# Optimization experiments

Measured on AMD Instinct MI355X. Metric: run time of the kernel, lower is better.

## Reference

```python
import jax, jax.numpy as jnp
from jax import lax
import numpy as np

B = 128          # batch size
S = 207          # input spatial size implied by outputSpatialSize=[8,8]
N_PTS = 256000
NEG = -1e30      # -inf stand-in for masked max-pooling
# BNReLU channel counts in execution order: 8 resnet blocks x (bn1, bn2), final resnet BN(32), last BN(64)
SIZES = [8,8,8,8,8,16,16,16,16,24,24,24,24,32,32,32,32,64]
OFF = np.cumsum([0] + SIZES)

WSHAPES = dict(conv0=(3,3,1,8),
               c1a=(3,3,8,8), c1b=(3,3,8,8), c2a=(3,3,8,8), c2b=(3,3,8,8),
               c3a=(3,3,8,16), c3b=(3,3,16,16), c3r=(3,3,8,16),
               c4a=(3,3,16,16), c4b=(3,3,16,16),
               c5a=(3,3,16,24), c5b=(3,3,24,24), c5r=(3,3,16,24),
               c6a=(3,3,24,24), c6b=(3,3,24,24),
               c7a=(3,3,24,32), c7b=(3,3,32,32), c7r=(3,3,24,32),
               c8a=(3,3,32,32), c8b=(3,3,32,32),
               conv_last=(5,5,32,64))

def _conv(x, w, stride, padding):
    return lax.conv_general_dilated(x, w, (stride, stride), padding,
                                    dimension_numbers=('NHWC', 'HWIO', 'NHWC'))

def _pool_max(x, win, stride, init):
    return lax.reduce_window(x, init, lax.max, (1, win, win, 1), (1, stride, stride, 1), 'VALID')

def _bnrelu(x, m, g, b):
    # eval-mode BN folded to affine, applied on active sites only (inactive stay exactly 0)
    return m * jax.nn.relu(x * g + b)

def _subconv(x, w, m):
    # submanifold conv == dense conv on zero-filled grid, output restricted to active sites
    return _conv(x, w, 1, 'SAME') * m

def _strided(x, w, m, win, stride):
    # scn.Convolution: output site active iff any active input in its receptive field
    m2 = _pool_max(m, win, stride, 0.0)
    return _conv(x, w, stride, 'VALID') * m2, m2

def _block(x, m, g1, b1, w1, g2, b2, w2, wres, stride):
    # pre-activation basic block from scn.SparseResNet
    h = _bnrelu(x, m, g1, b1)
    if stride == 1:
        h, m2 = _subconv(h, w1, m), m
    else:
        h, m2 = _strided(h, w1, m, 3, 2)
    h = _subconv(_bnrelu(h, m2, g2, b2), w2, m2)
    r = x if wres is None else _strided(x, wres, m, 3, 2)[0]
    return h + r, m2

def _forward(locations, batch_idx, features, bn_gamma, bn_beta, W):
    idx = (batch_idx, locations[:, 0], locations[:, 1], jnp.zeros_like(batch_idx))
    x = jnp.zeros((B, S, S, 1), jnp.float32).at[idx].add(features[:, 0])  # InputLayer (sum dups)
    m = jnp.zeros((B, S, S, 1), jnp.float32).at[idx].set(1.0)             # active-site mask
    g = [bn_gamma[OFF[i]:OFF[i+1]] for i in range(len(SIZES))]
    b = [bn_beta[OFF[i]:OFF[i+1]] for i in range(len(SIZES))]
    x = _subconv(x, W['conv0'], m)                              # 1->8 @ 207x207
    # MaxPooling(pool 3, stride 2) over active sites only
    m2 = _pool_max(m, 3, 2, 0.0)
    x = jnp.where(m2 > 0, _pool_max(jnp.where(m > 0, x, NEG), 3, 2, NEG), 0.0)
    m = m2                                                      # @ 103x103
    blocks = [('c1a', 'c1b', None, 1), ('c2a', 'c2b', None, 1),
              ('c3a', 'c3b', 'c3r', 2), ('c4a', 'c4b', None, 1),
              ('c5a', 'c5b', 'c5r', 2), ('c6a', 'c6b', None, 1),
              ('c7a', 'c7b', 'c7r', 2), ('c8a', 'c8b', None, 1)]
    for i, (k1, k2, kr, st) in enumerate(blocks):
        x, m = _block(x, m, g[2*i], b[2*i], W[k1], g[2*i+1], b[2*i+1], W[k2],
                      None if kr is None else W[kr], st)        # 103->51->25->12
    x = _bnrelu(x, m, g[16], b[16])                             # final resnet BNReLU(32)
    x, m = _strided(x, W['conv_last'], m, 5, 1)                 # 32->64, 12x12 -> 8x8
    x = _bnrelu(x, m, g[17], b[17])
    flat = x.transpose(0, 3, 1, 2).reshape(B, -1)               # SparseToDense + flatten (NCHW order)
    return (flat @ W['w_lin'].T).reshape(B, -1, 1)              # [B, 100, 1]

def setup_inputs():
    key = jax.random.key(0)
    ks = iter(jax.random.split(key, 64))
    inp = {
        'locations': jax.random.randint(next(ks), (N_PTS, 2), 0, S, dtype=jnp.int32),
        'batch_idx': jax.random.randint(next(ks), (N_PTS,), 0, B, dtype=jnp.int32),
        'features': jax.random.normal(next(ks), (N_PTS, 1), jnp.float32),
        'bn_gamma': 1.0 + 0.1 * jax.random.normal(next(ks), (int(OFF[-1]),), jnp.float32),
        'bn_beta': 0.1 * jax.random.normal(next(ks), (int(OFF[-1]),), jnp.float32),
    }
    for name, shp in WSHAPES.items():
        fan_in = int(np.prod(shp[:-1]))
        inp[name] = jax.random.normal(next(ks), shp, jnp.float32) * (2.0 / fan_in) ** 0.5
    inp['w_lin'] = jax.random.normal(next(ks), (100, 64 * 8 * 8), jnp.float32) * (1.0 / 4096.0) ** 0.5
    return inp

def reference(locations, batch_idx, features, bn_gamma, bn_beta, conv0,
              c1a, c1b, c2a, c2b, c3a, c3b, c3r, c4a, c4b, c5a, c5b, c5r,
              c6a, c6b, c7a, c7b, c7r, c8a, c8b, conv_last, w_lin):
    W = dict(conv0=conv0, c1a=c1a, c1b=c1b, c2a=c2a, c2b=c2b, c3a=c3a, c3b=c3b, c3r=c3r,
             c4a=c4a, c4b=c4b, c5a=c5a, c5b=c5b, c5r=c5r, c6a=c6a, c6b=c6b,
             c7a=c7a, c7b=c7b, c7r=c7r, c8a=c8a, c8b=c8b, conv_last=conv_last, w_lin=w_lin)
    return _forward(locations, batch_idx, features, bn_gamma, bn_beta, W)
```

## Files before the change

kernel.cpp:

```cpp
#include <hip/hip_runtime.h>

#define S 207
#define BATCH 128
#define NPTS 256000

static const int OFFS[19] = {0,8,16,24,32,40,56,72,88,104,128,152,176,200,232,264,296,328,392};

__global__ void zero2_kernel(float4* __restrict__ a, float4* __restrict__ b, int n4) {
    int i = blockIdx.x * blockDim.x + threadIdx.x;
    if (i < n4) { a[i] = make_float4(0,0,0,0); b[i] = make_float4(0,0,0,0); }
}

__global__ void zero_kernel(float* __restrict__ p, int n) {
    int i = blockIdx.x * blockDim.x + threadIdx.x;
    if (i < n) p[i] = 0.0f;
}

__global__ void scatter_kernel(const int* __restrict__ loc, const int* __restrict__ bidx,
                               const float* __restrict__ feat,
                               float* __restrict__ xs, float* __restrict__ ms) {
    int t = blockIdx.x * blockDim.x + threadIdx.x;
    if (t >= NPTS) return;
    int b = bidx[t];
    int r = loc[2 * t];
    int c = loc[2 * t + 1];
    int idx = (b * S + r) * S + c;
    atomicAdd(&xs[idx], feat[t]);
    ms[idx] = 1.0f;
}

__global__ __launch_bounds__(256) void conv0_pool_kernel(
    const float* __restrict__ xs, const float* __restrict__ ms,
    const float* __restrict__ w,
    float* __restrict__ x1, float* __restrict__ m1) {
    const int Hout = 103;
    int opix = blockIdx.x * 256 + threadIdx.x;
    int total = BATCH * Hout * Hout;
    if (opix >= total) return;
    int wo = opix % Hout;
    int t = opix / Hout;
    int ho = t % Hout;
    int b  = t / Hout;

    float mv[3][3];
    float mwin = 0.0f;
    #pragma unroll
    for (int pi = 0; pi < 3; ++pi)
        #pragma unroll
        for (int pj = 0; pj < 3; ++pj) {
            float m = ms[(b * S + 2 * ho + pi) * S + 2 * wo + pj];
            mv[pi][pj] = m;
            mwin = fmaxf(mwin, m);
        }
    float* xp = x1 + (size_t)opix * 8;
    if (mwin <= 0.0f) {
        *(float4*)xp = make_float4(0,0,0,0);
        *(float4*)(xp + 4) = make_float4(0,0,0,0);
        m1[opix] = 0.0f;
        return;
    }
    float p[5][5];
    #pragma unroll
    for (int r = 0; r < 5; ++r) {
        int ii = 2 * ho - 1 + r;
        #pragma unroll
        for (int c = 0; c < 5; ++c) {
            int jj = 2 * wo - 1 + c;
            bool ok = ((unsigned)ii < (unsigned)S) && ((unsigned)jj < (unsigned)S);
            p[r][c] = ok ? xs[(b * S + ii) * S + jj] : 0.0f;
        }
    }
    float best[8];
    #pragma unroll
    for (int co = 0; co < 8; ++co) best[co] = -1e30f;
    #pragma unroll
    for (int pi = 0; pi < 3; ++pi)
        #pragma unroll
        for (int pj = 0; pj < 3; ++pj) {
            if (mv[pi][pj] > 0.0f) {
                float acc[8];
                #pragma unroll
                for (int co = 0; co < 8; ++co) acc[co] = 0.0f;
                #pragma unroll
                for (int kh = 0; kh < 3; ++kh)
                    #pragma unroll
                    for (int kw = 0; kw < 3; ++kw) {
                        float x = p[pi + kh][pj + kw];
                        #pragma unroll
                        for (int co = 0; co < 8; ++co)
                            acc[co] = fmaf(x, w[(kh * 3 + kw) * 8 + co], acc[co]);
                    }
                #pragma unroll
                for (int co = 0; co < 8; ++co) best[co] = fmaxf(best[co], acc[co]);
            }
        }
    *(float4*)xp = make_float4(best[0], best[1], best[2], best[3]);
    *(float4*)(xp + 4) = make_float4(best[4], best[5], best[6], best[7]);
    m1[opix] = 1.0f;
}

template <int C, int TILE, int NTX>
__global__ __launch_bounds__(256) void resblock_kernel(
    const float* __restrict__ in, const float* __restrict__ mask,
    const float* __restrict__ w1, const float* __restrict__ w2,
    const float* __restrict__ g1, const float* __restrict__ bb1,
    const float* __restrict__ g2, const float* __restrict__ bb2,
    float* __restrict__ out, int H) {
    constexpr int XT = TILE + 4, HT = TILE + 2;
    constexpr int XA = XT * XT, HA = HT * HT;
    __shared__ float xs[C][XA];
    __shared__ float h1[C][HA];
    __shared__ float msh[XA];

    int tid = threadIdx.x;
    int bid = blockIdx.x;
    int b = bid / (NTX * NTX);
    int t = bid % (NTX * NTX);
    int r0 = (t / NTX) * TILE, c0 = (t % NTX) * TILE;

    float gr[C], br[C];
    #pragma unroll
    for (int c = 0; c < C; ++c) { gr[c] = g1[c]; br[c] = bb1[c]; }

    for (int i = tid; i < XA; i += 256) {
        int py = i / XT, px = i % XT;
        int gy = r0 - 2 + py, gx = c0 - 2 + px;
        bool ok = (unsigned)gy < (unsigned)H && (unsigned)gx < (unsigned)H;
        float m = 0.0f;
        if (ok) m = mask[(size_t)(b * H + gy) * H + gx];
        msh[i] = m;
        if (m > 0.0f) {
            const float* ip = in + ((size_t)(b * H + gy) * H + gx) * C;
            #pragma unroll
            for (int c = 0; c < C; ++c)
                xs[c][i] = m * fmaxf(fmaf(ip[c], gr[c], br[c]), 0.0f);
        } else {
            #pragma unroll
            for (int c = 0; c < C; ++c) xs[c][i] = 0.0f;
        }
    }
    #pragma unroll
    for (int c = 0; c < C; ++c) { gr[c] = g2[c]; br[c] = bb2[c]; }
    __syncthreads();

    for (int pos = tid; pos < HA; pos += 256) {
        int py = pos / HT, px = pos % HT;
        float mc = msh[(py + 1) * XT + px + 1];
        float acc[C];
        #pragma unroll
        for (int co = 0; co < C; ++co) acc[co] = 0.0f;
        if (mc > 0.0f) {
            #pragma unroll
            for (int kh = 0; kh < 3; ++kh)
                #pragma unroll
                for (int kw = 0; kw < 3; ++kw) {
                    int pix = (py + kh) * XT + px + kw;
                    const float* wp = w1 + (kh * 3 + kw) * C * C;
                    #pragma unroll
                    for (int ci = 0; ci < C; ++ci) {
                        float xv = xs[ci][pix];
                        #pragma unroll
                        for (int co = 0; co < C; ++co)
                            acc[co] = fmaf(xv, wp[ci * C + co], acc[co]);
                    }
                }
        }
        #pragma unroll
        for (int co = 0; co < C; ++co)
            h1[co][pos] = mc * fmaxf(fmaf(acc[co] * mc, gr[co], br[co]), 0.0f);
    }
    __syncthreads();

    {
        int ty = tid / TILE, tx = tid % TILE;
        int gy = r0 + ty, gx = c0 + tx;
        if (gy < H && gx < H) {
            float mo = msh[(ty + 2) * XT + tx + 2];
            float acc[C];
            #pragma unroll
            for (int co = 0; co < C; ++co) acc[co] = 0.0f;
            if (mo > 0.0f) {
                #pragma unroll
                for (int kh = 0; kh < 3; ++kh)
                    #pragma unroll
                    for (int kw = 0; kw < 3; ++kw) {
                        int pix = (ty + kh) * HT + tx + kw;
                        const float* wp = w2 + (kh * 3 + kw) * C * C;
                        #pragma unroll
                        for (int ci = 0; ci < C; ++ci) {
                            float xv = h1[ci][pix];
                            #pragma unroll
                            for (int co = 0; co < C; ++co)
                                acc[co] = fmaf(xv, wp[ci * C + co], acc[co]);
                        }
                    }
            }
            const float* rp = in + ((size_t)(b * H + gy) * H + gx) * C;
            float* op = out + ((size_t)(b * H + gy) * H + gx) * C;
            #pragma unroll
            for (int j = 0; j < C; j += 4) {
                float4 r4 = *(const float4*)(rp + j);
                float4 o4;
                o4.x = fmaf(acc[j],     mo, r4.x);
                o4.y = fmaf(acc[j + 1], mo, r4.y);
                o4.z = fmaf(acc[j + 2], mo, r4.z);
                o4.w = fmaf(acc[j + 3], mo, r4.w);
                *(float4*)(op + j) = o4;
            }
        }
    }
}

template <int K, int CIN, int COUT, int COT, bool BN, bool RES>
__global__ __launch_bounds__(256) void fconv_kernel(
    const float* __restrict__ in, const float* __restrict__ w,
    const float* __restrict__ g, const float* __restrict__ bbn,
    const float* __restrict__ mIn, const float* __restrict__ mOut,
    const float* __restrict__ res, float* __restrict__ out,
    int Hin, int Hout, int stride, int pad) {
    const int Win = Hin, Wout = Hout;
    int npix = BATCH * Hout * Wout;
    int opix = blockIdx.x * 256 + threadIdx.x;
    if (opix >= npix) return;
    int co0 = blockIdx.y * COT;
    int wo = opix % Wout;
    int t = opix / Wout;
    int ho = t % Hout;
    int b  = t / Hout;

    float mo = mOut[opix];
    float* op = out + (size_t)opix * COUT + co0;
    if (mo <= 0.0f) {
        #pragma unroll
        for (int j = 0; j < COT; j += 4) {
            float4 r4 = RES ? *(const float4*)(res + (size_t)opix * COUT + co0 + j)
                            : make_float4(0,0,0,0);
            *(float4*)(op + j) = r4;
        }
        return;
    }
    float acc[COT];
    #pragma unroll
    for (int j = 0; j < COT; ++j) acc[j] = 0.0f;

    #pragma unroll
    for (int kh = 0; kh < K; ++kh) {
        int ih = ho * stride + kh - pad;
        if ((unsigned)ih >= (unsigned)Hin) continue;
        #pragma unroll
        for (int kw = 0; kw < K; ++kw) {
            int iw = wo * stride + kw - pad;
            if ((unsigned)iw >= (unsigned)Win) continue;
            int ipix = (b * Hin + ih) * Win + iw;
            float mi = 1.0f;
            if (BN) { mi = mIn[ipix]; if (mi <= 0.0f) continue; }
            const float* ip = in + (size_t)ipix * CIN;
            const float* wp = w + (kh * K + kw) * CIN * COUT + co0;
            #pragma unroll
            for (int ci = 0; ci < CIN; ci += 4) {
                float4 xv = *(const float4*)(ip + ci);
                if (BN) {
                    xv.x = mi * fmaxf(fmaf(xv.x, g[ci],     bbn[ci]),     0.0f);
                    xv.y = mi * fmaxf(fmaf(xv.y, g[ci + 1], bbn[ci + 1]), 0.0f);
                    xv.z = mi * fmaxf(fmaf(xv.z, g[ci + 2], bbn[ci + 2]), 0.0f);
                    xv.w = mi * fmaxf(fmaf(xv.w, g[ci + 3], bbn[ci + 3]), 0.0f);
                }
                #pragma unroll
                for (int j = 0; j < COT; ++j) {
                    acc[j] = fmaf(xv.x, wp[(ci    ) * COUT + j], acc[j]);
                    acc[j] = fmaf(xv.y, wp[(ci + 1) * COUT + j], acc[j]);
                    acc[j] = fmaf(xv.z, wp[(ci + 2) * COUT + j], acc[j]);
                    acc[j] = fmaf(xv.w, wp[(ci + 3) * COUT + j], acc[j]);
                }
            }
        }
    }
    #pragma unroll
    for (int j = 0; j < COT; j += 4) {
        float4 o4;
        o4.x = acc[j] * mo; o4.y = acc[j+1] * mo; o4.z = acc[j+2] * mo; o4.w = acc[j+3] * mo;
        if (RES) {
            float4 r4 = *(const float4*)(res + (size_t)opix * COUT + co0 + j);
            o4.x += r4.x; o4.y += r4.y; o4.z += r4.z; o4.w += r4.w;
        }
        *(float4*)(op + j) = o4;
    }
}

template <int CIN, int COUT, int COT>
__global__ __launch_bounds__(256) void strided_ra_kernel(
    const float* __restrict__ in,
    const float* __restrict__ wR, const float* __restrict__ wA,
    const float* __restrict__ g, const float* __restrict__ bbn,
    const float* __restrict__ mIn, float* __restrict__ mOutBuf,
    float* __restrict__ outR, float* __restrict__ outA,
    int Hin, int Hout) {
    constexpr int NG = COUT / COT;
    int npix = BATCH * Hout * Hout;
    int opix = blockIdx.x * 256 + threadIdx.x;
    if (opix >= npix) return;
    int path = blockIdx.y / NG;
    int co0  = (blockIdx.y % NG) * COT;
    int wo = opix % Hout;
    int t = opix / Hout;
    int ho = t % Hout;
    int b  = t / Hout;

    const float* wsel = path ? wA : wR;
    float acc[COT];
    #pragma unroll
    for (int j = 0; j < COT; ++j) acc[j] = 0.0f;
    float m2 = 0.0f;

    #pragma unroll
    for (int kh = 0; kh < 3; ++kh) {
        int ih = 2 * ho + kh;
        #pragma unroll
        for (int kw = 0; kw < 3; ++kw) {
            int iw = 2 * wo + kw;
            int ipix = (b * Hin + ih) * Hin + iw;
            float mi = mIn[ipix];
            if (mi <= 0.0f) continue;
            m2 = fmaxf(m2, mi);
            const float* ip = in + (size_t)ipix * CIN;
            const float* wp = wsel + (kh * 3 + kw) * CIN * COUT + co0;
            #pragma unroll
            for (int ci = 0; ci < CIN; ci += 4) {
                float4 xv = *(const float4*)(ip + ci);
                if (path) {
                    xv.x = mi * fmaxf(fmaf(xv.x, g[ci],     bbn[ci]),     0.0f);
                    xv.y = mi * fmaxf(fmaf(xv.y, g[ci + 1], bbn[ci + 1]), 0.0f);
                    xv.z = mi * fmaxf(fmaf(xv.z, g[ci + 2], bbn[ci + 2]), 0.0f);
                    xv.w = mi * fmaxf(fmaf(xv.w, g[ci + 3], bbn[ci + 3]), 0.0f);
                }
                #pragma unroll
                for (int j = 0; j < COT; ++j) {
                    acc[j] = fmaf(xv.x, wp[(ci    ) * COUT + j], acc[j]);
                    acc[j] = fmaf(xv.y, wp[(ci + 1) * COUT + j], acc[j]);
                    acc[j] = fmaf(xv.z, wp[(ci + 2) * COUT + j], acc[j]);
                    acc[j] = fmaf(xv.w, wp[(ci + 3) * COUT + j], acc[j]);
                }
            }
        }
    }
    if (blockIdx.y == 0) mOutBuf[opix] = m2;
    float* op = (path ? outA : outR) + (size_t)opix * COUT + co0;
    #pragma unroll
    for (int j = 0; j < COT; j += 4) {
        float4 o4;
        o4.x = acc[j] * m2; o4.y = acc[j+1] * m2; o4.z = acc[j+2] * m2; o4.w = acc[j+3] * m2;
        *(float4*)(op + j) = o4;
    }
}

__global__ void pool_kernel(const float* __restrict__ in, float* __restrict__ out,
                            int Hin, int Win, int Hout, int Wout, int win, int stride) {
    int tid = blockIdx.x * blockDim.x + threadIdx.x;
    int total = BATCH * Hout * Wout;
    if (tid >= total) return;
    int wo = tid % Wout;
    int p = tid / Wout;
    int ho = p % Hout;
    int b  = p / Hout;
    float mx = 0.0f;
    for (int i = 0; i < win; ++i)
        for (int j = 0; j < win; ++j)
            mx = fmaxf(mx, in[(b * Hin + ho * stride + i) * Win + wo * stride + j]);
    out[tid] = mx;
}

__global__ __launch_bounds__(256) void bn_tr_kernel(
    const float* __restrict__ x, const float* __restrict__ m,
    const float* __restrict__ g, const float* __restrict__ bb,
    float* __restrict__ xt) {
    int tid = blockIdx.x * 256 + threadIdx.x;
    if (tid >= BATCH * 4096) return;
    int c = tid & 63, hw = (tid >> 6) & 63, b = tid >> 12;
    float v = m[b * 64 + hw] * fmaxf(fmaf(x[tid], g[c], bb[c]), 0.0f);
    xt[((size_t)b << 12) + c * 64 + hw] = v;
}

__global__ __launch_bounds__(256) void linear_gemm_kernel(
    const float* __restrict__ xt, const float* __restrict__ wl,
    float* __restrict__ out) {
    int o = blockIdx.x;
    int half = threadIdx.x >> 7;
    int b = threadIdx.x & 127;
    int k0 = blockIdx.y * 512 + half * 256;
    const float* xp = xt + ((size_t)b << 12) + k0;
    const float* wp = wl + o * 4096 + k0;
    float acc = 0.0f;
    #pragma unroll 16
    for (int k = 0; k < 256; k += 4) {
        float4 xv = *(const float4*)(xp + k);
        float4 wv = *(const float4*)(wp + k);
        acc = fmaf(xv.x, wv.x, acc); acc = fmaf(xv.y, wv.y, acc);
        acc = fmaf(xv.z, wv.z, acc); acc = fmaf(xv.w, wv.w, acc);
    }
    atomicAdd(&out[b * 100 + o], acc);
}

template <int K, int CIN, int COUT, int COT, bool BN, bool RES>
static inline void fconv(hipStream_t s, const float* in, const float* w,
                         const float* g, const float* bbn,
                         const float* mIn, const float* mOut, const float* res,
                         float* out, int Hin, int Hout, int stride, int pad) {
    int npix = BATCH * Hout * Hout;
    dim3 grid((npix + 255) / 256, COUT / COT);
    fconv_kernel<K, CIN, COUT, COT, BN, RES><<<grid, 256, 0, s>>>(
        in, w, g, bbn, mIn, mOut, res, out, Hin, Hout, stride, pad);
}

template <int CIN, int COUT, int COT>
static inline void strided_ra(hipStream_t s, const float* in, const float* wR, const float* wA,
                              const float* g, const float* bbn, const float* mIn,
                              float* mOutBuf, float* outR, float* outA, int Hin, int Hout) {
    int npix = BATCH * Hout * Hout;
    dim3 grid((npix + 255) / 256, 2 * (COUT / COT));
    strided_ra_kernel<CIN, COUT, COT><<<grid, 256, 0, s>>>(
        in, wR, wA, g, bbn, mIn, mOutBuf, outR, outA, Hin, Hout);
}

extern "C" void kernel_launch(void* const* d_in, const int* in_sizes, int n_in,
                              void* d_out, int out_size, void* d_ws, size_t ws_size,
                              hipStream_t stream) {
    const int*   loc   = (const int*)d_in[0];
    const int*   bidx  = (const int*)d_in[1];
    const float* feat  = (const float*)d_in[2];
    const float* gamma = (const float*)d_in[3];
    const float* beta  = (const float*)d_in[4];
    const float* Wconv0 = (const float*)d_in[5];
    const float* Wc1a = (const float*)d_in[6];
    const float* Wc1b = (const float*)d_in[7];
    const float* Wc2a = (const float*)d_in[8];
    const float* Wc2b = (const float*)d_in[9];
    const float* Wc3a = (const float*)d_in[10];
    const float* Wc3b = (const float*)d_in[11];
    const float* Wc3r = (const float*)d_in[12];
    const float* Wc4a = (const float*)d_in[13];
    const float* Wc4b = (const float*)d_in[14];
    const float* Wc5a = (const float*)d_in[15];
    const float* Wc5b = (const float*)d_in[16];
    const float* Wc5r = (const float*)d_in[17];
    const float* Wc6a = (const float*)d_in[18];
    const float* Wc6b = (const float*)d_in[19];
    const float* Wc7a = (const float*)d_in[20];
    const float* Wc7b = (const float*)d_in[21];
    const float* Wc7r = (const float*)d_in[22];
    const float* Wc8a = (const float*)d_in[23];
    const float* Wc8b = (const float*)d_in[24];
    const float* Wlast = (const float*)d_in[25];
    const float* wlin  = (const float*)d_in[26];

    const size_t SZB = (size_t)BATCH * 103 * 103 * 8;
    const size_t SZM = (size_t)BATCH * 103 * 103;
    float* b0 = (float*)d_ws;
    float* b1 = b0 + SZB;
    float* b2 = b1 + SZB;
    float* m0 = b2 + SZB;
    float* m1 = m0 + SZM;

    const float* G[18];
    const float* Bt[18];
    for (int i = 0; i < 18; ++i) { G[i] = gamma + OFFS[i]; Bt[i] = beta + OFFS[i]; }

    {
        int n = BATCH * S * S;
        zero2_kernel<<<(n / 4 + 255) / 256, 256, 0, stream>>>((float4*)b1, (float4*)b2, n / 4);
        scatter_kernel<<<(NPTS + 255) / 256, 256, 0, stream>>>(loc, bidx, feat, b1, b2);
        int total = BATCH * 103 * 103;
        conv0_pool_kernel<<<(total + 255) / 256, 256, 0, stream>>>(b1, b2, Wconv0, b0, m0);
    }

    resblock_kernel<8, 16, 7><<<dim3(7 * 7 * BATCH), 256, 0, stream>>>(
        b0, m0, Wc1a, Wc1b, G[0], Bt[0], G[1], Bt[1], b1, 103);
    resblock_kernel<8, 16, 7><<<dim3(7 * 7 * BATCH), 256, 0, stream>>>(
        b1, m0, Wc2a, Wc2b, G[2], Bt[2], G[3], Bt[3], b2, 103);
    strided_ra<8, 16, 16>(stream, b2, Wc3r, Wc3a, G[4], Bt[4], m0, m1, b0, b1, 103, 51);
    fconv<3, 16, 16, 8, true, true >(stream, b1, Wc3b, G[5], Bt[5], m1, m1, b0, b2, 51, 51, 1, 1);
    fconv<3, 16, 16, 8, true, false>(stream, b2, Wc4a, G[6], Bt[6], m1, m1, nullptr, b0, 51, 51, 1, 1);
    fconv<3, 16, 16, 8, true, true >(stream, b0, Wc4b, G[7], Bt[7], m1, m1, b2,      b1, 51, 51, 1, 1);
    strided_ra<16, 24, 24>(stream, b1, Wc5r, Wc5a, G[8], Bt[8], m1, m0, b0, b2, 51, 25);
    fconv<3, 24, 24, 8, true, true >(stream, b2, Wc5b, G[9], Bt[9], m0, m0, b0, b1, 25, 25, 1, 1);
    fconv<3, 24, 24, 8, true, false>(stream, b1, Wc6a, G[10], Bt[10], m0, m0, nullptr, b0, 25, 25, 1, 1);
    fconv<3, 24, 24, 8, true, true >(stream, b0, Wc6b, G[11], Bt[11], m0, m0, b1,      b2, 25, 25, 1, 1);
    strided_ra<24, 32, 8>(stream, b2, Wc7r, Wc7a, G[12], Bt[12], m0, m1, b0, b1, 25, 12);
    fconv<3, 32, 32, 4, true, true >(stream, b1, Wc7b, G[13], Bt[13], m1, m1, b0, b2, 12, 12, 1, 1);
    fconv<3, 32, 32, 4, true, false>(stream, b2, Wc8a, G[14], Bt[14], m1, m1, nullptr, b0, 12, 12, 1, 1);
    fconv<3, 32, 32, 4, true, true >(stream, b0, Wc8b, G[15], Bt[15], m1, m1, b2,      b1, 12, 12, 1, 1);
    pool_kernel<<<(BATCH * 64 + 255) / 256, 256, 0, stream>>>(m1, m0, 12, 12, 8, 8, 5, 1);
    fconv<5, 32, 64, 4, true, false>(stream, b1, Wlast, G[16], Bt[16], m1, m0, nullptr, b0, 12, 8, 1, 0);
    bn_tr_kernel<<<(BATCH * 4096 + 255) / 256, 256, 0, stream>>>(b0, m0, G[17], Bt[17], b2);
    zero_kernel<<<(BATCH * 100 + 255) / 256, 256, 0, stream>>>((float*)d_out, BATCH * 100);
    linear_gemm_kernel<<<dim3(100, 8), 256, 0, stream>>>(b2, wlin, (float*)d_out);
}
```

Before: 797.3 us.

## Batch conv input loads per row and add shared-memory tiled last conv

The generic and strided conv kernels now issue all input loads for a kernel row before computing, and use predicated zeroing instead of early continues, which gives more memory-level parallelism at the cost of more registers. The final 5x5 conv is replaced by a dedicated kernel that stages BN-ReLU'd input rows and weights in shared memory, split by kernel row across blocks. Its partial sums go to a buffer that the BN/transpose kernel reduces. The 51x51 layers also switch to a full 16-channel output tile, which removes redundant input reads. Trade-offs are the loads now issued for inactive neighbours, the larger partial buffer traffic, and some lost occupancy.

```diff
diff --git a/kernel.cpp b/kernel.cpp
--- a/kernel.cpp
+++ b/kernel.cpp
@@ -246,31 +246,52 @@
     #pragma unroll
     for (int kh = 0; kh < K; ++kh) {
         int ih = ho * stride + kh - pad;
-        if ((unsigned)ih >= (unsigned)Hin) continue;
+        bool rok = (unsigned)ih < (unsigned)Hin;
+        int ihc = rok ? ih : 0;
+        float mi[K];
+        float4 xv[K][CIN / 4];
         #pragma unroll
         for (int kw = 0; kw < K; ++kw) {
             int iw = wo * stride + kw - pad;
-            if ((unsigned)iw >= (unsigned)Win) continue;
-            int ipix = (b * Hin + ih) * Win + iw;
-            float mi = 1.0f;
-            if (BN) { mi = mIn[ipix]; if (mi <= 0.0f) continue; }
+            bool ok = rok && ((unsigned)iw < (unsigned)Win);
+            int ipix = (b * Hin + ihc) * Win + (ok ? iw : 0);
+            float m = mIn[ipix];
+            mi[kw] = ok ? m : 0.0f;
             const float* ip = in + (size_t)ipix * CIN;
+            #pragma unroll
+            for (int q = 0; q < CIN / 4; ++q) xv[kw][q] = *(const float4*)(ip + 4 * q);
+        }
+        #pragma unroll
+        for (int kw = 0; kw < K; ++kw) {
+            if (BN) {
+                bool on = mi[kw] > 0.0f;
+                #pragma unroll
+                for (int q = 0; q < CIN / 4; ++q) {
+                    int ci = 4 * q;
+                    float4& x4 = xv[kw][q];
+                    x4.x = on ? fmaxf(fmaf(x4.x, g[ci],     bbn[ci]),     0.0f) : 0.0f;
+                    x4.y = on ? fmaxf(fmaf(x4.y, g[ci + 1], bbn[ci + 1]), 0.0f) : 0.0f;
+                    x4.z = on ? fmaxf(fmaf(x4.z, g[ci + 2], bbn[ci + 2]), 0.0f) : 0.0f;
+                    x4.w = on ? fmaxf(fmaf(x4.w, g[ci + 3], bbn[ci + 3]), 0.0f) : 0.0f;
+                }
+            } else {
+                bool on = mi[kw] > 0.0f;
+                if (!on) {
+                    #pragma unroll
+                    for (int q = 0; q < CIN / 4; ++q) xv[kw][q] = make_float4(0,0,0,0);
+                }
+            }
             const float* wp = w + (kh * K + kw) * CIN * COUT + co0;
             #pragma unroll
-            for (int ci = 0; ci < CIN; ci += 4) {
-                float4 xv = *(const float4*)(ip + ci);
-                if (BN) {
-                    xv.x = mi * fmaxf(fmaf(xv.x, g[ci],     bbn[ci]),     0.0f);
-                    xv.y = mi * fmaxf(fmaf(xv.y, g[ci + 1], bbn[ci + 1]), 0.0f);
-                    xv.z = mi * fmaxf(fmaf(xv.z, g[ci + 2], bbn[ci + 2]), 0.0f);
-                    xv.w = mi * fmaxf(fmaf(xv.w, g[ci + 3], bbn[ci + 3]), 0.0f);
-                }
+            for (int q = 0; q < CIN / 4; ++q) {
+                float4 x4 = xv[kw][q];
+                int ci = 4 * q;
                 #pragma unroll
                 for (int j = 0; j < COT; ++j) {
-                    acc[j] = fmaf(xv.x, wp[(ci    ) * COUT + j], acc[j]);
-                    acc[j] = fmaf(xv.y, wp[(ci + 1) * COUT + j], acc[j]);
-                    acc[j] = fmaf(xv.z, wp[(ci + 2) * COUT + j], acc[j]);
-                    acc[j] = fmaf(xv.w, wp[(ci + 3) * COUT + j], acc[j]);
+                    acc[j] = fmaf(x4.x, wp[(ci    ) * COUT + j], acc[j]);
+                    acc[j] = fmaf(x4.y, wp[(ci + 1) * COUT + j], acc[j]);
+                    acc[j] = fmaf(x4.z, wp[(ci + 2) * COUT + j], acc[j]);
+                    acc[j] = fmaf(x4.w, wp[(ci + 3) * COUT + j], acc[j]);
                 }
             }
         }
@@ -315,30 +336,44 @@
     #pragma unroll
     for (int kh = 0; kh < 3; ++kh) {
         int ih = 2 * ho + kh;
+        float mi[3];
+        float4 xv[3][CIN / 4];
         #pragma unroll
         for (int kw = 0; kw < 3; ++kw) {
             int iw = 2 * wo + kw;
             int ipix = (b * Hin + ih) * Hin + iw;
-            float mi = mIn[ipix];
-            if (mi <= 0.0f) continue;
-            m2 = fmaxf(m2, mi);
+            mi[kw] = mIn[ipix];
             const float* ip = in + (size_t)ipix * CIN;
+            #pragma unroll
+            for (int q = 0; q < CIN / 4; ++q) xv[kw][q] = *(const float4*)(ip + 4 * q);
+        }
+        #pragma unroll
+        for (int kw = 0; kw < 3; ++kw) {
+            float m = mi[kw];
+            m2 = fmaxf(m2, m);
+            if (path) {
+                bool on = m > 0.0f;
+                #pragma unroll
+                for (int q = 0; q < CIN / 4; ++q) {
+                    int ci = 4 * q;
+                    float4& x4 = xv[kw][q];
+                    x4.x = on ? fmaxf(fmaf(x4.x, g[ci],     bbn[ci]),     0.0f) : 0.0f;
+                    x4.y = on ? fmaxf(fmaf(x4.y, g[ci + 1], bbn[ci + 1]), 0.0f) : 0.0f;
+                    x4.z = on ? fmaxf(fmaf(x4.z, g[ci + 2], bbn[ci + 2]), 0.0f) : 0.0f;
+                    x4.w = on ? fmaxf(fmaf(x4.w, g[ci + 3], bbn[ci + 3]), 0.0f) : 0.0f;
+                }
+            }
             const float* wp = wsel + (kh * 3 + kw) * CIN * COUT + co0;
             #pragma unroll
-            for (int ci = 0; ci < CIN; ci += 4) {
-                float4 xv = *(const float4*)(ip + ci);
-                if (path) {
-                    xv.x = mi * fmaxf(fmaf(xv.x, g[ci],     bbn[ci]),     0.0f);
-                    xv.y = mi * fmaxf(fmaf(xv.y, g[ci + 1], bbn[ci + 1]), 0.0f);
-                    xv.z = mi * fmaxf(fmaf(xv.z, g[ci + 2], bbn[ci + 2]), 0.0f);
-                    xv.w = mi * fmaxf(fmaf(xv.w, g[ci + 3], bbn[ci + 3]), 0.0f);
-                }
+            for (int q = 0; q < CIN / 4; ++q) {
+                float4 x4 = xv[kw][q];
+                int ci = 4 * q;
                 #pragma unroll
                 for (int j = 0; j < COT; ++j) {
-                    acc[j] = fmaf(xv.x, wp[(ci    ) * COUT + j], acc[j]);
-                    acc[j] = fmaf(xv.y, wp[(ci + 1) * COUT + j], acc[j]);
-                    acc[j] = fmaf(xv.z, wp[(ci + 2) * COUT + j], acc[j]);
-                    acc[j] = fmaf(xv.w, wp[(ci + 3) * COUT + j], acc[j]);
+                    acc[j] = fmaf(x4.x, wp[(ci    ) * COUT + j], acc[j]);
+                    acc[j] = fmaf(x4.y, wp[(ci + 1) * COUT + j], acc[j]);
+                    acc[j] = fmaf(x4.z, wp[(ci + 2) * COUT + j], acc[j]);
+                    acc[j] = fmaf(x4.w, wp[(ci + 3) * COUT + j], acc[j]);
                 }
             }
         }
@@ -351,6 +386,78 @@
         o4.x = acc[j] * m2; o4.y = acc[j+1] * m2; o4.z = acc[j+2] * m2; o4.w = acc[j+3] * m2;
         *(float4*)(op + j) = o4;
     }
+}
+
+__global__ __launch_bounds__(256) void convlast_kernel(
+    const float* __restrict__ in,
+    const float* __restrict__ w,
+    const float* __restrict__ g, const float* __restrict__ bb,
+    const float* __restrict__ mIn,
+    float* __restrict__ part) {
+    __shared__ float xs[32 * 97];
+    __shared__ float ws[5 * 32 * 64];
+    int b   = blockIdx.x;
+    int kh  = blockIdx.y;
+    int tid = threadIdx.x;
+    for (int i = tid; i < 8 * 12 * 32; i += 256) {
+        int ci = i & 31;
+        int p  = i >> 5;
+        int gpix = (b * 12 + kh + p / 12) * 12 + (p % 12);
+        float m = mIn[gpix];
+        float v = 0.0f;
+        if (m > 0.0f) v = fmaxf(fmaf(in[(size_t)gpix * 32 + ci], g[ci], bb[ci]), 0.0f);
+        xs[ci * 97 + p] = v;
+    }
+    {
+        const float4* src = (const float4*)(w + kh * (5 * 32 * 64));
+        float4* dst = (float4*)ws;
+        for (int i = tid; i < 5 * 32 * 64 / 4; i += 256) dst[i] = src[i];
+    }
+    __syncthreads();
+
+    int px = tid & 63;
+    int cg = tid >> 6;
+    int ho = px >> 3, wo = px & 7;
+    float acc[16];
+    #pragma unroll
+    for (int j = 0; j < 16; ++j) acc[j] = 0.0f;
+    #pragma unroll
+    for (int kw = 0; kw < 5; ++kw) {
+        const float* xp = xs + ho * 12 + wo + kw;
+        const float* wp = ws + kw * (32 * 64) + cg * 16;
+        #pragma unroll
+        for (int ci = 0; ci < 32; ++ci) {
+            float xv = xp[ci * 97];
+            const float* wr = wp + ci * 64;
+            #pragma unroll
+            for (int j = 0; j < 16; j += 4) {
+                float4 w4 = *(const float4*)(wr + j);
+                acc[j]     = fmaf(xv, w4.x, acc[j]);
+                acc[j + 1] = fmaf(xv, w4.y, acc[j + 1]);
+                acc[j + 2] = fmaf(xv, w4.z, acc[j + 2]);
+                acc[j + 3] = fmaf(xv, w4.w, acc[j + 3]);
+            }
+        }
+    }
+    float* op = part + ((((size_t)kh * BATCH + b) * 64 + px) * 64) + cg * 16;
+    #pragma unroll
+    for (int j = 0; j < 16; j += 4)
+        *(float4*)(op + j) = make_float4(acc[j], acc[j+1], acc[j+2], acc[j+3]);
+}
+
+__global__ __launch_bounds__(256) void bn_tr_kernel(
+    const float* __restrict__ part, const float* __restrict__ m,
+    const float* __restrict__ g, const float* __restrict__ bb,
+    float* __restrict__ xt) {
+    int tid = blockIdx.x * 256 + threadIdx.x;
+    if (tid >= BATCH * 4096) return;
+    int c = tid & 63, hw = (tid >> 6) & 63, b = tid >> 12;
+    float s = 0.0f;
+    #pragma unroll
+    for (int k = 0; k < 5; ++k)
+        s += part[(((size_t)k * BATCH + b) * 64 + hw) * 64 + c];
+    float v = m[b * 64 + hw] * fmaxf(fmaf(s, g[c], bb[c]), 0.0f);
+    xt[((size_t)b << 12) + c * 64 + hw] = v;
 }
 
 __global__ void pool_kernel(const float* __restrict__ in, float* __restrict__ out,
@@ -367,17 +474,6 @@
         for (int j = 0; j < win; ++j)
             mx = fmaxf(mx, in[(b * Hin + ho * stride + i) * Win + wo * stride + j]);
     out[tid] = mx;
-}
-
-__global__ __launch_bounds__(256) void bn_tr_kernel(
-    const float* __restrict__ x, const float* __restrict__ m,
-    const float* __restrict__ g, const float* __restrict__ bb,
-    float* __restrict__ xt) {
-    int tid = blockIdx.x * 256 + threadIdx.x;
-    if (tid >= BATCH * 4096) return;
-    int c = tid & 63, hw = (tid >> 6) & 63, b = tid >> 12;
-    float v = m[b * 64 + hw] * fmaxf(fmaf(x[tid], g[c], bb[c]), 0.0f);
-    xt[((size_t)b << 12) + c * 64 + hw] = v;
 }
 
 __global__ __launch_bounds__(256) void linear_gemm_kernel(
@@ -477,9 +573,9 @@
     resblock_kernel<8, 16, 7><<<dim3(7 * 7 * BATCH), 256, 0, stream>>>(
         b1, m0, Wc2a, Wc2b, G[2], Bt[2], G[3], Bt[3], b2, 103);
     strided_ra<8, 16, 16>(stream, b2, Wc3r, Wc3a, G[4], Bt[4], m0, m1, b0, b1, 103, 51);
-    fconv<3, 16, 16, 8, true, true >(stream, b1, Wc3b, G[5], Bt[5], m1, m1, b0, b2, 51, 51, 1, 1);
-    fconv<3, 16, 16, 8, true, false>(stream, b2, Wc4a, G[6], Bt[6], m1, m1, nullptr, b0, 51, 51, 1, 1);
-    fconv<3, 16, 16, 8, true, true >(stream, b0, Wc4b, G[7], Bt[7], m1, m1, b2,      b1, 51, 51, 1, 1);
+    fconv<3, 16, 16, 16, true, true >(stream, b1, Wc3b, G[5], Bt[5], m1, m1, b0, b2, 51, 51, 1, 1);
+    fconv<3, 16, 16, 16, true, false>(stream, b2, Wc4a, G[6], Bt[6], m1, m1, nullptr, b0, 51, 51, 1, 1);
+    fconv<3, 16, 16, 16, true, true >(stream, b0, Wc4b, G[7], Bt[7], m1, m1, b2,      b1, 51, 51, 1, 1);
     strided_ra<16, 24, 24>(stream, b1, Wc5r, Wc5a, G[8], Bt[8], m1, m0, b0, b2, 51, 25);
     fconv<3, 24, 24, 8, true, true >(stream, b2, Wc5b, G[9], Bt[9], m0, m0, b0, b1, 25, 25, 1, 1);
     fconv<3, 24, 24, 8, true, false>(stream, b1, Wc6a, G[10], Bt[10], m0, m0, nullptr, b0, 25, 25, 1, 1);
@@ -489,7 +585,7 @@
     fconv<3, 32, 32, 4, true, false>(stream, b2, Wc8a, G[14], Bt[14], m1, m1, nullptr, b0, 12, 12, 1, 1);
     fconv<3, 32, 32, 4, true, true >(stream, b0, Wc8b, G[15], Bt[15], m1, m1, b2,      b1, 12, 12, 1, 1);
     pool_kernel<<<(BATCH * 64 + 255) / 256, 256, 0, stream>>>(m1, m0, 12, 12, 8, 8, 5, 1);
-    fconv<5, 32, 64, 4, true, false>(stream, b1, Wlast, G[16], Bt[16], m1, m0, nullptr, b0, 12, 8, 1, 0);
+    convlast_kernel<<<dim3(BATCH, 5), 256, 0, stream>>>(b1, Wlast, G[16], Bt[16], m1, b0);
     bn_tr_kernel<<<(BATCH * 4096 + 255) / 256, 256, 0, stream>>>(b0, m0, G[17], Bt[17], b2);
     zero_kernel<<<(BATCH * 100 + 255) / 256, 256, 0, stream>>>((float*)d_out, BATCH * 100);
     linear_gemm_kernel<<<dim3(100, 8), 256, 0, stream>>>(b2, wlin, (float*)d_out);
```

Measured after the change: 2.184 ms. 174% more time.

## Replace final 5x5 conv with LDS-tiled split-kernel-row kernel and fused reduction

Applied to the files above, without the earlier changes.

Adds a dedicated kernel for the last 5x5 convolution (32 to 64 channels, 12x12 to 8x8). Each block handles one batch image and one kernel row, staging the BN-ReLU activations and that row's weights in shared memory. It writes five partial sums, which the BN/transpose kernel then reduces before applying the final BN-ReLU and mask. The aim is more parallelism and more data reuse than the generic fconv path gives. The cost is extra global traffic for the five partial buffers, and the partials need b0 to be large enough to hold them.

```diff
diff --git a/kernel.cpp b/kernel.cpp
--- a/kernel.cpp
+++ b/kernel.cpp
@@ -353,6 +353,78 @@
     }
 }
 
+__global__ __launch_bounds__(256) void convlast_kernel(
+    const float* __restrict__ in,
+    const float* __restrict__ w,
+    const float* __restrict__ g, const float* __restrict__ bb,
+    const float* __restrict__ mIn,
+    float* __restrict__ part) {
+    __shared__ float xs[32 * 97];
+    __shared__ float ws[5 * 32 * 64];
+    int b   = blockIdx.x;
+    int kh  = blockIdx.y;
+    int tid = threadIdx.x;
+    for (int i = tid; i < 8 * 12 * 32; i += 256) {
+        int ci = i & 31;
+        int p  = i >> 5;
+        int gpix = (b * 12 + kh + p / 12) * 12 + (p % 12);
+        float m = mIn[gpix];
+        float v = 0.0f;
+        if (m > 0.0f) v = fmaxf(fmaf(in[(size_t)gpix * 32 + ci], g[ci], bb[ci]), 0.0f);
+        xs[ci * 97 + p] = v;
+    }
+    {
+        const float4* src = (const float4*)(w + kh * (5 * 32 * 64));
+        float4* dst = (float4*)ws;
+        for (int i = tid; i < 5 * 32 * 64 / 4; i += 256) dst[i] = src[i];
+    }
+    __syncthreads();
+
+    int px = tid & 63;
+    int cg = tid >> 6;
+    int ho = px >> 3, wo = px & 7;
+    float acc[16];
+    #pragma unroll
+    for (int j = 0; j < 16; ++j) acc[j] = 0.0f;
+    #pragma unroll
+    for (int kw = 0; kw < 5; ++kw) {
+        const float* xp = xs + ho * 12 + wo + kw;
+        const float* wp = ws + kw * (32 * 64) + cg * 16;
+        #pragma unroll
+        for (int ci = 0; ci < 32; ++ci) {
+            float xv = xp[ci * 97];
+            const float* wr = wp + ci * 64;
+            #pragma unroll
+            for (int j = 0; j < 16; j += 4) {
+                float4 w4 = *(const float4*)(wr + j);
+                acc[j]     = fmaf(xv, w4.x, acc[j]);
+                acc[j + 1] = fmaf(xv, w4.y, acc[j + 1]);
+                acc[j + 2] = fmaf(xv, w4.z, acc[j + 2]);
+                acc[j + 3] = fmaf(xv, w4.w, acc[j + 3]);
+            }
+        }
+    }
+    float* op = part + ((((size_t)kh * BATCH + b) * 64 + px) * 64) + cg * 16;
+    #pragma unroll
+    for (int j = 0; j < 16; j += 4)
+        *(float4*)(op + j) = make_float4(acc[j], acc[j+1], acc[j+2], acc[j+3]);
+}
+
+__global__ __launch_bounds__(256) void bn_tr_kernel(
+    const float* __restrict__ part, const float* __restrict__ m,
+    const float* __restrict__ g, const float* __restrict__ bb,
+    float* __restrict__ xt) {
+    int tid = blockIdx.x * 256 + threadIdx.x;
+    if (tid >= BATCH * 4096) return;
+    int c = tid & 63, hw = (tid >> 6) & 63, b = tid >> 12;
+    float s = 0.0f;
+    #pragma unroll
+    for (int k = 0; k < 5; ++k)
+        s += part[(((size_t)k * BATCH + b) * 64 + hw) * 64 + c];
+    float v = m[b * 64 + hw] * fmaxf(fmaf(s, g[c], bb[c]), 0.0f);
+    xt[((size_t)b << 12) + c * 64 + hw] = v;
+}
+
 __global__ void pool_kernel(const float* __restrict__ in, float* __restrict__ out,
                             int Hin, int Win, int Hout, int Wout, int win, int stride) {
     int tid = blockIdx.x * blockDim.x + threadIdx.x;
@@ -367,17 +439,6 @@
         for (int j = 0; j < win; ++j)
             mx = fmaxf(mx, in[(b * Hin + ho * stride + i) * Win + wo * stride + j]);
     out[tid] = mx;
-}
-
-__global__ __launch_bounds__(256) void bn_tr_kernel(
-    const float* __restrict__ x, const float* __restrict__ m,
-    const float* __restrict__ g, const float* __restrict__ bb,
-    float* __restrict__ xt) {
-    int tid = blockIdx.x * 256 + threadIdx.x;
-    if (tid >= BATCH * 4096) return;
-    int c = tid & 63, hw = (tid >> 6) & 63, b = tid >> 12;
-    float v = m[b * 64 + hw] * fmaxf(fmaf(x[tid], g[c], bb[c]), 0.0f);
-    xt[((size_t)b << 12) + c * 64 + hw] = v;
 }
 
 __global__ __launch_bounds__(256) void linear_gemm_kernel(
@@ -489,7 +550,7 @@
     fconv<3, 32, 32, 4, true, false>(stream, b2, Wc8a, G[14], Bt[14], m1, m1, nullptr, b0, 12, 12, 1, 1);
     fconv<3, 32, 32, 4, true, true >(stream, b0, Wc8b, G[15], Bt[15], m1, m1, b2,      b1, 12, 12, 1, 1);
     pool_kernel<<<(BATCH * 64 + 255) / 256, 256, 0, stream>>>(m1, m0, 12, 12, 8, 8, 5, 1);
-    fconv<5, 32, 64, 4, true, false>(stream, b1, Wlast, G[16], Bt[16], m1, m0, nullptr, b0, 12, 8, 1, 0);
+    convlast_kernel<<<dim3(BATCH, 5), 256, 0, stream>>>(b1, Wlast, G[16], Bt[16], m1, b0);
     bn_tr_kernel<<<(BATCH * 4096 + 255) / 256, 256, 0, stream>>>(b0, m0, G[17], Bt[17], b2);
     zero_kernel<<<(BATCH * 100 + 255) / 256, 256, 0, stream>>>((float*)d_out, BATCH * 100);
     linear_gemm_kernel<<<dim3(100, 8), 256, 0, stream>>>(b2, wlin, (float*)d_out);
```

New measurement: 766.2 us. 3.9% less time.
